# Kernel optimization log

Measured on AMD Instinct MI355X. Metric: run time of the kernel, lower is better.

## Reference

```python
import jax, jax.numpy as jnp
import numpy as np

B, H_IMG, W_IMG, K = 4, 60, 80, 8
HW = H_IMG * W_IMG
IMG_D, PT_D = 192, 128
NH, DH = 6, 64
INNER = NH * DH
NHF = 6
POS_D = 2 * (2 * NHF + 1)  # harmonic emb of 2-d offset, append_input=True -> 26
MAX_DIST = 0.1


def setup_inputs() -> dict:
    key = jax.random.key(0)
    ks = jax.random.split(key, 6)
    ys, xs = jnp.meshgrid(jnp.linspace(0.0, 1.0, H_IMG), jnp.linspace(0.0, 1.0, W_IMG), indexing='ij')
    img_uv = jnp.stack([xs.reshape(-1), ys.reshape(-1)], axis=-1)  # [HW, 2], normalized pixel grid
    return {
        'feat_2d': jax.random.normal(ks[0], (B, HW, IMG_D), jnp.float32),
        'feat_3d': jax.random.normal(ks[1], (B, HW, PT_D), jnp.float32),
        'proj_uv': jax.random.uniform(ks[2], (B, HW, 2), dtype=jnp.float32),
        'img_uv': img_uv,
        'ln_gamma': jnp.ones((IMG_D,), jnp.float32),
        'q_gamma': jnp.ones((NH, DH), jnp.float32),
        'k_gamma': jnp.ones((NH, DH), jnp.float32),
        'Wq': jax.random.normal(ks[3], (IMG_D, INNER), jnp.float32) * IMG_D ** -0.5,
        'Wkv': jax.random.normal(ks[4], (PT_D + POS_D, 2 * INNER), jnp.float32) * (PT_D + POS_D) ** -0.5,
        'Wout': jax.random.normal(ks[5], (INNER, INNER), jnp.float32) * INNER ** -0.5,
    }


def _layernorm(x, g, eps=1e-5):
    mu = jnp.mean(x, -1, keepdims=True)
    var = jnp.mean((x - mu) ** 2, -1, keepdims=True)
    return (x - mu) * jax.lax.rsqrt(var + eps) * g


def _rmsnorm(x, g):
    # lucidrains-style query/key RMSNorm: l2-normalize last dim, scale by sqrt(dim) * per-head gamma
    n = jnp.maximum(jnp.linalg.norm(x, axis=-1, keepdims=True), 1e-12)
    return x / n * (DH ** 0.5) * g


def reference(feat_2d, feat_3d, proj_uv, img_uv, ln_gamma, q_gamma, k_gamma, Wq, Wkv, Wout):
    # --- kNN: for each image pixel, k nearest projected points (brute force) ---
    d2 = (jnp.sum(img_uv ** 2, -1)[None, :, None]
          + jnp.sum(proj_uv ** 2, -1)[:, None, :]
          - 2.0 * jnp.einsum('qd,bnd->bqn', img_uv, proj_uv))  # [B, HW, HW]
    idx = jax.lax.top_k(-d2, K)[1]  # [B, HW, K] int32 indices

    # --- gather neighbor uv coords and 3d features ---
    knn_uv = img_uv[idx]                                        # [B, HW, K, 2]
    knn_f3 = jnp.take_along_axis(feat_3d, idx.reshape(B, HW * K, 1), axis=1).reshape(B, HW, K, PT_D)
    offset = knn_uv - img_uv[None, :, None, :]                  # [B, HW, K, 2]
    mask = jnp.sum(offset ** 2, -1) <= MAX_DIST ** 2            # [B, HW, K]

    # --- harmonic positional embedding of offsets ---
    freqs = 2.0 ** jnp.arange(NHF, dtype=jnp.float32)
    e = (offset[..., None] * freqs).reshape(B, HW, K, 2 * NHF)
    pos = jnp.concatenate([jnp.sin(e), jnp.cos(e), offset], -1)  # [B, HW, K, 26]

    # --- Q / K / V projections ---
    q = (_layernorm(feat_2d, ln_gamma) @ Wq).reshape(B, HW, NH, DH)
    kv = jnp.concatenate([knn_f3, pos], -1) @ Wkv               # [B, HW, K, 2*INNER]
    k_, v_ = jnp.split(kv, 2, axis=-1)
    k_ = k_.reshape(B, HW, K, NH, DH)
    v_ = v_.reshape(B, HW, K, NH, DH)
    q = _rmsnorm(q, q_gamma)
    k_ = _rmsnorm(k_, k_gamma)

    # --- tiny per-pixel attention (query len 1, key len K), scale=1.0 ---
    scores = jnp.einsum('bnhd,bnkhd->bnhk', q, k_)              # [B, HW, NH, K]
    scores = jnp.where(mask[:, :, None, :], scores, -1e30)
    attn = jax.nn.softmax(scores, axis=-1)
    out = jnp.einsum('bnhk,bnkhd->bnhd', attn, v_).reshape(B, HW, INNER)
    return out @ Wout  # output_type='1d': [B, HW, INNER]
```

## Files before the change

### kernel.cpp

```cpp
#include <hip/hip_runtime.h>
#include <math.h>

#define B_    4
#define HW_   4800
#define K_    8
#define IMGD  192
#define PTD   128
#define NH_   6
#define DH_   64
#define INNER 384
#define KVIN  154
#define QT    8
#define NJ    64
#define XBS   168
#define AST   392
#define KTQ   6
#define KTK   5
#define KTO   12

typedef _Float16 f16;
typedef __attribute__((ext_vector_type(8))) _Float16 f16x8;
typedef __attribute__((ext_vector_type(4))) float f32x4;

__global__ __launch_bounds__(256) void pack_kernel(
    const float* __restrict__ Wq, const float* __restrict__ Wkv,
    const float* __restrict__ Wout, f16* __restrict__ pw)
{
  const int e = blockIdx.x * 256 + threadIdx.x;
  if (e >= 672 * 512) return;
  const int f = e >> 9, r = e & 511, l = r >> 3, j = r & 7;
  const int lm = l & 15, kin = (l >> 4) * 8 + j;
  float v;
  if (f < 144) {
    const int nt = f / 6, kt = f % 6;
    v = Wq[(size_t)(kt * 32 + kin) * INNER + nt * 16 + lm];
  } else if (f < 264) {
    const int g = f - 144, nt = g / 5, kt = g % 5, k = kt * 32 + kin;
    v = (k < KVIN) ? Wkv[(size_t)k * (2 * INNER) + nt * 16 + lm] : 0.f;
  } else if (f < 384) {
    const int g = f - 264, nt = g / 5, kt = g % 5, k = kt * 32 + kin;
    v = (k < KVIN) ? Wkv[(size_t)k * (2 * INNER) + INNER + nt * 16 + lm] : 0.f;
  } else {
    const int g = f - 384, nt = g / 12, kt = g % 12;
    v = Wout[(size_t)(kt * 32 + kin) * INNER + nt * 16 + lm];
  }
  pw[e] = (f16)v;
}

#define KNN_INIT(d, ind)                                                      \
  _Pragma("unroll") for (int s = 0; s < K_; ++s) { d[s] = 3.4e38f; ind[s] = 0x7fffffff; }

#define KNN_INSERT(dd, n, dist, ind)                                          \
  if (dd < dist[K_ - 1]) {                                                    \
    bool placed = false;                                                      \
    _Pragma("unroll") for (int s = K_ - 1; s >= 1; --s) {                     \
      if (!placed) {                                                          \
        if (dd < dist[s - 1]) { dist[s] = dist[s - 1]; ind[s] = ind[s - 1]; } \
        else                  { dist[s] = dd; ind[s] = n; placed = true; }    \
      }                                                                       \
    }                                                                         \
    if (!placed) { dist[0] = dd; ind[0] = n; }                                \
  }

#define KNN_MERGE(dist, ind, qidx)                                            \
  _Pragma("unroll") for (int r = 0; r < K_; ++r) {                            \
    float hd = dist[0]; int hi = ind[0];                                      \
    float bd = hd; int bi = hi;                                               \
    _Pragma("unroll") for (int m = 1; m < 64; m <<= 1) {                      \
      float od = __shfl_xor(bd, m); int oi = __shfl_xor(bi, m);               \
      if (od < bd || (od == bd && oi < bi)) { bd = od; bi = oi; }             \
    }                                                                         \
    const bool won = (hd == bd && hi == bi);                                  \
    _Pragma("unroll") for (int s = 0; s < K_ - 1; ++s) {                      \
      dist[s] = won ? dist[s + 1] : dist[s];                                  \
      ind[s]  = won ? ind[s + 1]  : ind[s];                                   \
    }                                                                         \
    dist[K_ - 1] = won ? 3.4e38f : dist[K_ - 1];                              \
    ind[K_ - 1]  = won ? 0x7fffffff : ind[K_ - 1];                            \
    if (lane == r) idx_out[((size_t)b * HW_ + (qidx)) * K_ + r] = bi;         \
  }

__global__ __launch_bounds__(256) void knn_kernel(
    const float* __restrict__ proj_uv,
    const float* __restrict__ img_uv,
    int* __restrict__ idx_out)
{
#pragma clang fp contract(off)
  __shared__ float2 s_p[HW_];

  const int tid  = threadIdx.x;
  const int wave = tid >> 6;
  const int lane = tid & 63;
  const int blk  = blockIdx.x;
  const int b    = blk / (HW_ / 16);
  const int q0   = (blk % (HW_ / 16)) * 16 + wave * 4;

  const float2* pv = reinterpret_cast<const float2*>(proj_uv + (size_t)b * HW_ * 2);
  for (int i = tid; i < HW_; i += 256) s_p[i] = pv[i];
  __syncthreads();

  float qx[4], qy[4], sqq[4];
#pragma unroll
  for (int c = 0; c < 4; ++c) {
    qx[c] = img_uv[(q0 + c) * 2];
    qy[c] = img_uv[(q0 + c) * 2 + 1];
    sqq[c] = qx[c] * qx[c] + qy[c] * qy[c];
  }

  float dA[K_], dB[K_], dC[K_], dD[K_];
  int   iA[K_], iB[K_], iC[K_], iD[K_];
  KNN_INIT(dA, iA); KNN_INIT(dB, iB); KNN_INIT(dC, iC); KNN_INIT(dD, iD);

  for (int n = lane; n < HW_; n += 64) {
    const float2 p = s_p[n];
    const float sqp = p.x * p.x + p.y * p.y;
    const float t0 = fmaf(qy[0], p.y, qx[0] * p.x);
    const float e0 = (sqq[0] + sqp) - 2.0f * t0;
    KNN_INSERT(e0, n, dA, iA);
    const float t1 = fmaf(qy[1], p.y, qx[1] * p.x);
    const float e1 = (sqq[1] + sqp) - 2.0f * t1;
    KNN_INSERT(e1, n, dB, iB);
    const float t2 = fmaf(qy[2], p.y, qx[2] * p.x);
    const float e2 = (sqq[2] + sqp) - 2.0f * t2;
    KNN_INSERT(e2, n, dC, iC);
    const float t3 = fmaf(qy[3], p.y, qx[3] * p.x);
    const float e3 = (sqq[3] + sqp) - 2.0f * t3;
    KNN_INSERT(e3, n, dD, iD);
  }

  KNN_MERGE(dA, iA, q0 + 0);
  KNN_MERGE(dB, iB, q0 + 1);
  KNN_MERGE(dC, iC, q0 + 2);
  KNN_MERGE(dD, iD, q0 + 3);
}

__global__ __launch_bounds__(256, 4) void fused_kernel(
    const float* __restrict__ feat_2d,
    const float* __restrict__ feat_3d,
    const float* __restrict__ img_uv,
    const float* __restrict__ ln_gamma,
    const float* __restrict__ q_gamma,
    const float* __restrict__ k_gamma,
    const f16*   __restrict__ pw,
    const int*   __restrict__ idx_ws,
    float* __restrict__ out)
{
  __shared__ alignas(16) f16   s_X[NJ][XBS];
  __shared__ alignas(16) float s_regA[QT * AST];
  __shared__ float s_scores[NJ][NH_];
  __shared__ float s_kss[NJ][NH_];
  __shared__ float s_ksc[NJ][NH_];
  __shared__ float s_mask[NJ];
  __shared__ int   s_idx[NJ];
  __shared__ float s_offx[NJ];
  __shared__ float s_offy[NJ];
  __shared__ float s_norm[QT * NH_];

  f16* s_f16 = reinterpret_cast<f16*>(s_regA);
  float (*s_attn)[NH_][K_] = reinterpret_cast<float (*)[NH_][K_]>(&s_kss[0][0]);

  const int tid = threadIdx.x;
  const int b   = blockIdx.y;
  const int bx  = (blockIdx.x & 7) * 75 + (blockIdx.x >> 3);
  const int q0  = bx * QT;
  const int l   = tid & 63;
  const int w   = tid >> 6;
  const int lm  = l & 15;
  const int lg  = l >> 4;

  const f16* pwq = pw;
  const f16* pwk = pw + 144 * 512;
  const f16* pwv = pw + 264 * 512;
  const f16* pwo = pw + 384 * 512;

  if (tid < NJ) {
    const int j  = tid;
    const int q  = q0 + (j >> 3);
    const int id = idx_ws[((size_t)b * HW_ + q) * K_ + (j & 7)];
    s_idx[j] = id;
    const float ax = img_uv[id * 2], ay = img_uv[id * 2 + 1];
    const float bx2 = img_uv[q * 2], by2 = img_uv[q * 2 + 1];
    s_offx[j] = ax - bx2; s_offy[j] = ay - by2;
    const double dox = (double)ax - (double)bx2;
    const double doy = (double)ay - (double)by2;
    s_mask[j] = (dox * dox + doy * doy <= 0.010000000000000002) ? 1.f : 0.f;
  }
  {
    unsigned* z = (unsigned*)(s_f16 + 8 * AST);
    for (int o = tid; o < 4 * AST; o += 256) z[o] = 0u;
  }
  {
    const int r  = ((tid >> 6) << 1) | ((tid >> 5) & 1);
    const int sl = tid & 31;
    const float* row = feat_2d + ((size_t)b * HW_ + q0 + r) * IMGD;
    float x[6]; float sum = 0.f, ssq = 0.f;
#pragma unroll
    for (int i = 0; i < 6; ++i) { x[i] = row[sl + 32 * i]; sum += x[i]; ssq += x[i] * x[i]; }
#pragma unroll
    for (int m = 16; m >= 1; m >>= 1) { sum += __shfl_xor(sum, m); ssq += __shfl_xor(ssq, m); }
    const float mu = sum * (1.f / 192.f);
    float var = ssq * (1.f / 192.f) - mu * mu;
    var = fmaxf(var, 0.f);
    const float rstd = rsqrtf(var + 1e-5f);
#pragma unroll
    for (int i = 0; i < 6; ++i) {
      const int c = sl + 32 * i;
      s_f16[r * AST + c] = (f16)((x[i] - mu) * rstd * ln_gamma[c]);
    }
  }
  __syncthreads();

  const int jX = tid >> 2, tsub = tid & 3;
  float4 xf[8];
  {
    const float4* f4 = reinterpret_cast<const float4*>(
        feat_3d + ((size_t)b * HW_ + s_idx[jX]) * PTD) + tsub * 8;
#pragma unroll
    for (int i = 0; i < 8; ++i) xf[i] = f4[i];
  }
  f32x4 qacc[6];
#pragma unroll
  for (int t = 0; t < 6; ++t) qacc[t] = (f32x4){0.f, 0.f, 0.f, 0.f};
  {
    const f16* ar = s_f16 + lm * AST + lg * 8;
#pragma unroll
    for (int kt = 0; kt < KTQ; ++kt) {
      const f16x8 a = *(const f16x8*)(ar + kt * 32);
#pragma unroll
      for (int t = 0; t < 6; ++t) {
        const int nt = w * 6 + t;
        const f16x8 bf = *(const f16x8*)(pwq + (((nt * 6 + kt) << 6) + l) * 8);
        qacc[t] = __builtin_amdgcn_mfma_f32_16x16x32_f16(a, bf, qacc[t], 0, 0, 0);
      }
    }
  }
  {
    f16* xr = &s_X[jX][tsub * 32];
#pragma unroll
    for (int i = 0; i < 8; ++i) {
      xr[i * 4 + 0] = (f16)xf[i].x; xr[i * 4 + 1] = (f16)xf[i].y;
      xr[i * 4 + 2] = (f16)xf[i].z; xr[i * 4 + 3] = (f16)xf[i].w;
    }
    if (tsub == 0) {
      const float ox = s_offx[jX], oy = s_offy[jX];
      f16* xp = &s_X[jX][PTD];
#pragma unroll
      for (int m = 0; m < 6; ++m) {
        const float fr = (float)(1 << m);
        float sx, cx, sy, cy;
        sincosf(ox * fr, &sx, &cx);
        sincosf(oy * fr, &sy, &cy);
        xp[m] = (f16)sx; xp[6 + m] = (f16)sy;
        xp[12 + m] = (f16)cx; xp[18 + m] = (f16)cy;
      }
      xp[24] = (f16)ox; xp[25] = (f16)oy;
#pragma unroll
      for (int m = 26; m < 32; ++m) xp[m] = (f16)0.f;
    }
  }
  __syncthreads();

  if (lg < 2) {
#pragma unroll
    for (int t = 0; t < 6; ++t) {
#pragma unroll
      for (int reg = 0; reg < 4; ++reg) {
        s_regA[(lg * 4 + reg) * AST + (w * 6 + t) * 16 + lm] = qacc[t][reg];
      }
    }
  }
  __syncthreads();

  if (tid < QT * NH_) {
    const int r = tid / NH_, h = tid % NH_;
    const float* v = s_regA + r * AST + h * DH_;
    float ss = 0.f;
#pragma unroll
    for (int d = 0; d < DH_; ++d) ss += v[d] * v[d];
    s_norm[tid] = fmaxf(sqrtf(ss), 1e-12f);
  }
  __syncthreads();

  {
    const int r  = tid >> 5;
    const int c0 = (tid & 31) * 12;
#pragma unroll
    for (int i = 0; i < 12; ++i) {
      const int c = c0 + i;
      const float n = s_norm[r * NH_ + (c >> 6)];
      s_regA[r * AST + c] *= (8.f / n) * q_gamma[c];
    }
  }
  for (int o = tid; o < NJ * NH_; o += 256) {
    s_kss[o / NH_][o % NH_] = 0.f;
    s_ksc[o / NH_][o % NH_] = 0.f;
  }
  __syncthreads();

  {
    for (int h = 0; h < NH_; ++h) {
      const int nt  = h * 4 + w;
      const int col = nt * 16 + lm;
      f16x8 bf[KTK];
#pragma unroll
      for (int kt = 0; kt < KTK; ++kt)
        bf[kt] = *(const f16x8*)(pwk + (((nt * KTK + kt) << 6) + l) * 8);
      const float kg = k_gamma[col];
#pragma unroll
      for (int mt = 0; mt < 4; ++mt) {
        const f16* xh = &s_X[16 * mt + lm][lg * 8];
        f32x4 c = (f32x4){0.f, 0.f, 0.f, 0.f};
#pragma unroll
        for (int kt = 0; kt < KTK; ++kt)
          c = __builtin_amdgcn_mfma_f32_16x16x32_f16(
              *(const f16x8*)(xh + kt * 32), bf[kt], c, 0, 0, 0);
        const int rq = 2 * mt + (lg >> 1);
        const float qg = s_regA[rq * AST + col] * kg;
        float ss[4], sc[4];
#pragma unroll
        for (int reg = 0; reg < 4; ++reg) {
          const float v = c[reg];
          ss[reg] = v * v; sc[reg] = v * qg;
        }
#pragma unroll
        for (int m = 1; m < 16; m <<= 1) {
#pragma unroll
          for (int reg = 0; reg < 4; ++reg) {
            ss[reg] += __shfl_xor(ss[reg], m);
            sc[reg] += __shfl_xor(sc[reg], m);
          }
        }
        if (lm == 0) {
#pragma unroll
          for (int reg = 0; reg < 4; ++reg) {
            const int row = 16 * mt + 4 * lg + reg;
            atomicAdd(&s_kss[row][h], ss[reg]);
            atomicAdd(&s_ksc[row][h], sc[reg]);
          }
        }
      }
    }
  }
  __syncthreads();
  for (int o = tid; o < NJ * NH_; o += 256) {
    const int row = o / NH_, h = o - row * NH_;
    const float nn = fmaxf(sqrtf(s_kss[row][h]), 1e-12f);
    s_scores[row][h] = (8.f / nn) * s_ksc[row][h];
  }
  __syncthreads();

  if (tid < QT * NH_) {
    const int r = tid / NH_, h = tid % NH_;
    float s[K_]; float mx = -1e38f;
#pragma unroll
    for (int k = 0; k < K_; ++k) {
      float v = s_scores[r * K_ + k][h];
      if (s_mask[r * K_ + k] == 0.f) v = -1e30f;
      s[k] = v; mx = fmaxf(mx, v);
    }
    float sum = 0.f;
#pragma unroll
    for (int k = 0; k < K_; ++k) { const float pp = expf(s[k] - mx); s[k] = pp; sum += pp; }
    const float inv = 1.f / sum;
#pragma unroll
    for (int k = 0; k < K_; ++k) s_attn[r][h][k] = s[k] * inv;
  }
  __syncthreads();

  {
    unsigned* z = (unsigned*)(s_f16 + 8 * AST);
    for (int o = tid; o < 4 * AST; o += 256) z[o] = 0u;
  }
  {
    const int k0 = (lg & 1) * 4;
#pragma unroll
    for (int t = 0; t < 6; ++t) {
      const int nt = w * 6 + t;
      const int h  = nt >> 2;
      f16x8 bf[KTK];
#pragma unroll
      for (int kt = 0; kt < KTK; ++kt)
        bf[kt] = *(const f16x8*)(pwv + (((nt * KTK + kt) << 6) + l) * 8);
#pragma unroll
      for (int mt = 0; mt < 4; ++mt) {
        const f16* xh = &s_X[16 * mt + lm][lg * 8];
        f32x4 c = (f32x4){0.f, 0.f, 0.f, 0.f};
#pragma unroll
        for (int kt = 0; kt < KTK; ++kt)
          c = __builtin_amdgcn_mfma_f32_16x16x32_f16(
              *(const f16x8*)(xh + kt * 32), bf[kt], c, 0, 0, 0);
        const int qrow = 2 * mt + (lg >> 1);
        const float4 at = *(const float4*)&s_attn[qrow][h][k0];
        float p = at.x * c[0] + at.y * c[1] + at.z * c[2] + at.w * c[3];
        p += __shfl_xor(p, 16);
        if ((lg & 1) == 0) s_f16[qrow * AST + nt * 16 + lm] = (f16)p;
      }
    }
  }
  __syncthreads();

  {
    f32x4 oacc[6];
#pragma unroll
    for (int t = 0; t < 6; ++t) oacc[t] = (f32x4){0.f, 0.f, 0.f, 0.f};
    const f16* ar = s_f16 + lm * AST + lg * 8;
#pragma unroll
    for (int kt = 0; kt < KTO; ++kt) {
      const f16x8 a = *(const f16x8*)(ar + kt * 32);
#pragma unroll
      for (int t = 0; t < 6; ++t) {
        const int nt = w * 6 + t;
        const f16x8 bf = *(const f16x8*)(pwo + (((nt * 12 + kt) << 6) + l) * 8);
        oacc[t] = __builtin_amdgcn_mfma_f32_16x16x32_f16(a, bf, oacc[t], 0, 0, 0);
      }
    }
    if (lg < 2) {
      float* orow0 = out + ((size_t)b * HW_ + q0) * INNER;
#pragma unroll
      for (int reg = 0; reg < 4; ++reg) {
        const int m = lg * 4 + reg;
#pragma unroll
        for (int t = 0; t < 6; ++t) {
          orow0[(size_t)m * INNER + (w * 6 + t) * 16 + lm] = oacc[t][reg];
        }
      }
    }
  }
}

extern "C" void kernel_launch(void* const* d_in, const int* in_sizes, int n_in,
                              void* d_out, int out_size, void* d_ws, size_t ws_size,
                              hipStream_t stream) {
  (void)in_sizes; (void)n_in; (void)out_size; (void)ws_size;
  const float* feat_2d = (const float*)d_in[0];
  const float* feat_3d = (const float*)d_in[1];
  const float* proj_uv = (const float*)d_in[2];
  const float* img_uv  = (const float*)d_in[3];
  const float* ln_g    = (const float*)d_in[4];
  const float* q_g     = (const float*)d_in[5];
  const float* k_g     = (const float*)d_in[6];
  const float* Wq      = (const float*)d_in[7];
  const float* Wkv     = (const float*)d_in[8];
  const float* Wout    = (const float*)d_in[9];
  float* out = (float*)d_out;

  int* idx_ws = (int*)d_ws;
  f16* pw = (f16*)((char*)d_ws + 614400);

  pack_kernel<<<dim3(1344), 256, 0, stream>>>(Wq, Wkv, Wout, pw);
  knn_kernel<<<dim3(B_ * HW_ / 16), 256, 0, stream>>>(proj_uv, img_uv, idx_ws);
  fused_kernel<<<dim3(HW_ / QT, B_), 256, 0, stream>>>(
      feat_2d, feat_3d, img_uv, ln_g, q_g, k_g, pw, idx_ws, out);
}
```

Measured before the change: 316.2 us.

## Fold weight packing into kNN kernel, fuse q-norm, and apply attention before V projection

```diff
diff --git a/kernel.cpp b/kernel.cpp
--- a/kernel.cpp
+++ b/kernel.cpp
@@ -22,31 +22,6 @@
 typedef __attribute__((ext_vector_type(8))) _Float16 f16x8;
 typedef __attribute__((ext_vector_type(4))) float f32x4;
 
-__global__ __launch_bounds__(256) void pack_kernel(
-    const float* __restrict__ Wq, const float* __restrict__ Wkv,
-    const float* __restrict__ Wout, f16* __restrict__ pw)
-{
-  const int e = blockIdx.x * 256 + threadIdx.x;
-  if (e >= 672 * 512) return;
-  const int f = e >> 9, r = e & 511, l = r >> 3, j = r & 7;
-  const int lm = l & 15, kin = (l >> 4) * 8 + j;
-  float v;
-  if (f < 144) {
-    const int nt = f / 6, kt = f % 6;
-    v = Wq[(size_t)(kt * 32 + kin) * INNER + nt * 16 + lm];
-  } else if (f < 264) {
-    const int g = f - 144, nt = g / 5, kt = g % 5, k = kt * 32 + kin;
-    v = (k < KVIN) ? Wkv[(size_t)k * (2 * INNER) + nt * 16 + lm] : 0.f;
-  } else if (f < 384) {
-    const int g = f - 264, nt = g / 5, kt = g % 5, k = kt * 32 + kin;
-    v = (k < KVIN) ? Wkv[(size_t)k * (2 * INNER) + INNER + nt * 16 + lm] : 0.f;
-  } else {
-    const int g = f - 384, nt = g / 12, kt = g % 12;
-    v = Wout[(size_t)(kt * 32 + kin) * INNER + nt * 16 + lm];
-  }
-  pw[e] = (f16)v;
-}
-
 #define KNN_INIT(d, ind)                                                      \
   _Pragma("unroll") for (int s = 0; s < K_; ++s) { d[s] = 3.4e38f; ind[s] = 0x7fffffff; }
 
@@ -80,9 +55,11 @@
     if (lane == r) idx_out[((size_t)b * HW_ + (qidx)) * K_ + r] = bi;         \
   }
 
-__global__ __launch_bounds__(256) void knn_kernel(
+__global__ __launch_bounds__(512) void knn_kernel(
     const float* __restrict__ proj_uv,
     const float* __restrict__ img_uv,
+    const float* __restrict__ Wq, const float* __restrict__ Wkv,
+    const float* __restrict__ Wout, f16* __restrict__ pw,
     int* __restrict__ idx_out)
 {
 #pragma clang fp contract(off)
@@ -92,11 +69,31 @@
   const int wave = tid >> 6;
   const int lane = tid & 63;
   const int blk  = blockIdx.x;
-  const int b    = blk / (HW_ / 16);
-  const int q0   = (blk % (HW_ / 16)) * 16 + wave * 4;
+  const int b    = blk / (HW_ / 32);
+  const int q0   = (blk % (HW_ / 32)) * 32 + wave * 4;
+
+  for (int e = blk * 512 + tid; e < 672 * 512; e += 600 * 512) {
+    const int f = e >> 9, r = e & 511, l = r >> 3, j = r & 7;
+    const int lm = l & 15, kin = (l >> 4) * 8 + j;
+    float v;
+    if (f < 144) {
+      const int nt = f / 6, kt = f % 6;
+      v = Wq[(size_t)(kt * 32 + kin) * INNER + nt * 16 + lm];
+    } else if (f < 264) {
+      const int g = f - 144, nt = g / 5, kt = g % 5, k = kt * 32 + kin;
+      v = (k < KVIN) ? Wkv[(size_t)k * (2 * INNER) + nt * 16 + lm] : 0.f;
+    } else if (f < 384) {
+      const int g = f - 264, nt = g / 5, kt = g % 5, k = kt * 32 + kin;
+      v = (k < KVIN) ? Wkv[(size_t)k * (2 * INNER) + INNER + nt * 16 + lm] : 0.f;
+    } else {
+      const int g = f - 384, nt = g / 12, kt = g % 12;
+      v = Wout[(size_t)(kt * 32 + kin) * INNER + nt * 16 + lm];
+    }
+    pw[e] = (f16)v;
+  }
 
   const float2* pv = reinterpret_cast<const float2*>(proj_uv + (size_t)b * HW_ * 2);
-  for (int i = tid; i < HW_; i += 256) s_p[i] = pv[i];
+  for (int i = tid; i < HW_; i += 512) s_p[i] = pv[i];
   __syncthreads();
 
   float qx[4], qy[4], sqq[4];
@@ -147,17 +144,16 @@
 {
   __shared__ alignas(16) f16   s_X[NJ][XBS];
   __shared__ alignas(16) float s_regA[QT * AST];
-  __shared__ float s_scores[NJ][NH_];
-  __shared__ float s_kss[NJ][NH_];
-  __shared__ float s_ksc[NJ][NH_];
+  __shared__ alignas(16) float s_attn[QT][NH_][K_];
+  __shared__ alignas(16) float s_kss[NJ][NH_];
+  __shared__ alignas(16) float s_ksc[NJ][NH_];
+  __shared__ float s_qss[QT][NH_];
   __shared__ float s_mask[NJ];
   __shared__ int   s_idx[NJ];
   __shared__ float s_offx[NJ];
   __shared__ float s_offy[NJ];
-  __shared__ float s_norm[QT * NH_];
 
   f16* s_f16 = reinterpret_cast<f16*>(s_regA);
-  float (*s_attn)[NH_][K_] = reinterpret_cast<float (*)[NH_][K_]>(&s_kss[0][0]);
 
   const int tid = threadIdx.x;
   const int b   = blockIdx.y;
@@ -189,6 +185,11 @@
     unsigned* z = (unsigned*)(s_f16 + 8 * AST);
     for (int o = tid; o < 4 * AST; o += 256) z[o] = 0u;
   }
+  if (tid < QT * NH_) s_qss[tid / NH_][tid % NH_] = 0.f;
+  for (int o = tid; o < NJ * NH_; o += 256) {
+    s_kss[o / NH_][o % NH_] = 0.f;
+    s_ksc[o / NH_][o % NH_] = 0.f;
+  }
   {
     const int r  = ((tid >> 6) << 1) | ((tid >> 5) & 1);
     const int sl = tid & 31;
@@ -258,46 +259,31 @@
       for (int m = 26; m < 32; ++m) xp[m] = (f16)0.f;
     }
   }
-  __syncthreads();
-
   if (lg < 2) {
+    const int h0w = (w * 6) >> 2;
+    float s2a[4], s2b[4];
+#pragma unroll
+    for (int reg = 0; reg < 4; ++reg) { s2a[reg] = 0.f; s2b[reg] = 0.f; }
 #pragma unroll
     for (int t = 0; t < 6; ++t) {
+      const int hi = ((w * 6 + t) >> 2) - h0w;
 #pragma unroll
       for (int reg = 0; reg < 4; ++reg) {
-        s_regA[(lg * 4 + reg) * AST + (w * 6 + t) * 16 + lm] = qacc[t][reg];
-      }
-    }
-  }
-  __syncthreads();
-
-  if (tid < QT * NH_) {
-    const int r = tid / NH_, h = tid % NH_;
-    const float* v = s_regA + r * AST + h * DH_;
-    float ss = 0.f;
-#pragma unroll
-    for (int d = 0; d < DH_; ++d) ss += v[d] * v[d];
-    s_norm[tid] = fmaxf(sqrtf(ss), 1e-12f);
-  }
-  __syncthreads();
-
-  {
-    const int r  = tid >> 5;
-    const int c0 = (tid & 31) * 12;
-#pragma unroll
-    for (int i = 0; i < 12; ++i) {
-      const int c = c0 + i;
-      const float n = s_norm[r * NH_ + (c >> 6)];
-      s_regA[r * AST + c] *= (8.f / n) * q_gamma[c];
-    }
-  }
-  for (int o = tid; o < NJ * NH_; o += 256) {
-    s_kss[o / NH_][o % NH_] = 0.f;
-    s_ksc[o / NH_][o % NH_] = 0.f;
-  }
-  __syncthreads();
-
-  {
+        const float v = qacc[t][reg];
+        s_regA[(lg * 4 + reg) * AST + (w * 6 + t) * 16 + lm] = v;
+        if (hi == 0) s2a[reg] += v * v; else s2b[reg] += v * v;
+      }
+    }
+#pragma unroll
+    for (int reg = 0; reg < 4; ++reg) {
+      atomicAdd(&s_qss[lg * 4 + reg][h0w], s2a[reg]);
+      atomicAdd(&s_qss[lg * 4 + reg][h0w + 1], s2b[reg]);
+    }
+  }
+  __syncthreads();
+
+  {
+#pragma unroll
     for (int h = 0; h < NH_; ++h) {
       const int nt  = h * 4 + w;
       const int col = nt * 16 + lm;
@@ -305,7 +291,7 @@
 #pragma unroll
       for (int kt = 0; kt < KTK; ++kt)
         bf[kt] = *(const f16x8*)(pwk + (((nt * KTK + kt) << 6) + l) * 8);
-      const float kg = k_gamma[col];
+      const float gg = k_gamma[col] * q_gamma[col];
 #pragma unroll
       for (int mt = 0; mt < 4; ++mt) {
         const f16* xh = &s_X[16 * mt + lm][lg * 8];
@@ -315,7 +301,8 @@
           c = __builtin_amdgcn_mfma_f32_16x16x32_f16(
               *(const f16x8*)(xh + kt * 32), bf[kt], c, 0, 0, 0);
         const int rq = 2 * mt + (lg >> 1);
-        const float qg = s_regA[rq * AST + col] * kg;
+        const float nnq = fmaxf(sqrtf(s_qss[rq][h]), 1e-12f);
+        const float qg = s_regA[rq * AST + col] * (8.f / nnq) * gg;
         float ss[4], sc[4];
 #pragma unroll
         for (int reg = 0; reg < 4; ++reg) {
@@ -342,20 +329,16 @@
     }
   }
   __syncthreads();
-  for (int o = tid; o < NJ * NH_; o += 256) {
-    const int row = o / NH_, h = o - row * NH_;
-    const float nn = fmaxf(sqrtf(s_kss[row][h]), 1e-12f);
-    s_scores[row][h] = (8.f / nn) * s_ksc[row][h];
-  }
-  __syncthreads();
 
   if (tid < QT * NH_) {
     const int r = tid / NH_, h = tid % NH_;
     float s[K_]; float mx = -1e38f;
 #pragma unroll
     for (int k = 0; k < K_; ++k) {
-      float v = s_scores[r * K_ + k][h];
-      if (s_mask[r * K_ + k] == 0.f) v = -1e30f;
+      const int row = r * K_ + k;
+      const float nn = fmaxf(sqrtf(s_kss[row][h]), 1e-12f);
+      float v = (8.f / nn) * s_ksc[row][h];
+      if (s_mask[row] == 0.f) v = -1e30f;
       s[k] = v; mx = fmaxf(mx, v);
     }
     float sum = 0.f;
@@ -371,29 +354,68 @@
     unsigned* z = (unsigned*)(s_f16 + 8 * AST);
     for (int o = tid; o < 4 * AST; o += 256) z[o] = 0u;
   }
-  {
-    const int k0 = (lg & 1) * 4;
-#pragma unroll
-    for (int t = 0; t < 6; ++t) {
-      const int nt = w * 6 + t;
-      const int h  = nt >> 2;
-      f16x8 bf[KTK];
+  f16x8 xbv[4];
+#pragma unroll
+  for (int rep = 0; rep < 4; ++rep) {
+    const int task = tid + 256 * rep;
+    if (task < 960) {
+      const int p = task / 320, rem = task - p * 320;
+      const int r16 = rem / 20, cb = rem - r16 * 20;
+      const int q = r16 & 7, hh = 2 * p + (r16 >> 3);
+      const float4 a0 = *(const float4*)&s_attn[q][hh][0];
+      const float4 a1 = *(const float4*)&s_attn[q][hh][4];
+      const float av[8] = {a0.x, a0.y, a0.z, a0.w, a1.x, a1.y, a1.z, a1.w};
+      float acc[8];
+#pragma unroll
+      for (int e = 0; e < 8; ++e) acc[e] = 0.f;
+#pragma unroll
+      for (int k = 0; k < 8; ++k) {
+        const f16x8 xv = *(const f16x8*)&s_X[q * 8 + k][cb * 8];
+#pragma unroll
+        for (int e = 0; e < 8; ++e) acc[e] += av[k] * (float)xv[e];
+      }
+      f16x8 rr;
+#pragma unroll
+      for (int e = 0; e < 8; ++e) rr[e] = (f16)acc[e];
+      xbv[rep] = rr;
+    }
+  }
+  __syncthreads();
+#pragma unroll
+  for (int rep = 0; rep < 4; ++rep) {
+    const int task = tid + 256 * rep;
+    if (task < 960) {
+      const int p = task / 320, rem = task - p * 320;
+      const int r16 = rem / 20, cb = rem - r16 * 20;
+      *(f16x8*)&s_X[p * 16 + r16][cb * 8] = xbv[rep];
+    }
+  }
+  __syncthreads();
+
+  {
+#pragma unroll
+    for (int p = 0; p < 3; ++p) {
+      f16x8 af[KTK];
 #pragma unroll
       for (int kt = 0; kt < KTK; ++kt)
-        bf[kt] = *(const f16x8*)(pwv + (((nt * KTK + kt) << 6) + l) * 8);
-#pragma unroll
-      for (int mt = 0; mt < 4; ++mt) {
-        const f16* xh = &s_X[16 * mt + lm][lg * 8];
+        af[kt] = *(const f16x8*)&s_X[p * 16 + lm][lg * 8 + kt * 32];
+#pragma unroll
+      for (int ii = 0; ii < 2; ++ii) {
+        const int nt = w + 4 * (2 * p + ii);
+        const int h  = nt >> 2;
         f32x4 c = (f32x4){0.f, 0.f, 0.f, 0.f};
 #pragma unroll
-        for (int kt = 0; kt < KTK; ++kt)
-          c = __builtin_amdgcn_mfma_f32_16x16x32_f16(
-              *(const f16x8*)(xh + kt * 32), bf[kt], c, 0, 0, 0);
-        const int qrow = 2 * mt + (lg >> 1);
-        const float4 at = *(const float4*)&s_attn[qrow][h][k0];
-        float p = at.x * c[0] + at.y * c[1] + at.z * c[2] + at.w * c[3];
-        p += __shfl_xor(p, 16);
-        if ((lg & 1) == 0) s_f16[qrow * AST + nt * 16 + lm] = (f16)p;
+        for (int kt = 0; kt < KTK; ++kt) {
+          const f16x8 bf = *(const f16x8*)(pwv + (((nt * KTK + kt) << 6) + l) * 8);
+          c = __builtin_amdgcn_mfma_f32_16x16x32_f16(af[kt], bf, c, 0, 0, 0);
+        }
+        if ((lg >> 1) == (h & 1)) {
+#pragma unroll
+          for (int reg = 0; reg < 4; ++reg) {
+            const int q = (lg * 4 + reg) & 7;
+            s_f16[q * AST + nt * 16 + lm] = (f16)c[reg];
+          }
+        }
       }
     }
   }
@@ -447,8 +469,8 @@
   int* idx_ws = (int*)d_ws;
   f16* pw = (f16*)((char*)d_ws + 614400);
 
-  pack_kernel<<<dim3(1344), 256, 0, stream>>>(Wq, Wkv, Wout, pw);
-  knn_kernel<<<dim3(B_ * HW_ / 16), 256, 0, stream>>>(proj_uv, img_uv, idx_ws);
+  knn_kernel<<<dim3(B_ * HW_ / 32), 512, 0, stream>>>(
+      proj_uv, img_uv, Wq, Wkv, Wout, pw, idx_ws);
   fused_kernel<<<dim3(HW_ / QT, B_), 256, 0, stream>>>(
       feat_2d, feat_3d, img_uv, ln_g, q_g, k_g, pw, idx_ws, out);
 }
```

Result: slower. 329.2 us (+4.1%).
